# Optimization experiments

Measured on AMD Instinct MI355X. Metric: run time of the kernel, lower is better.

## Reference

```python
import jax, jax.numpy as jnp
import numpy as np


def setup_inputs() -> dict:
    key = jax.random.key(0)
    ks = jax.random.split(key, 6)
    B, H, T, Dk, Dv = 64, 16, 4, 128, 256
    q = jax.random.normal(ks[0], (B, H, T, Dk), dtype=jnp.float32)
    k = jax.random.normal(ks[1], (B, H, T, Dk), dtype=jnp.float32)
    v = jax.random.normal(ks[2], (B, H, T, Dv), dtype=jnp.float32)
    g = jax.random.uniform(ks[3], (B, H, T), dtype=jnp.float32)
    beta = jax.random.uniform(ks[4], (B, H, T), dtype=jnp.float32)
    last_recurrent_state = jax.random.normal(ks[5], (B, H, Dk, Dv), dtype=jnp.float32)
    return {"q": q, "k": k, "v": v, "g": g, "beta": beta,
            "last_recurrent_state": last_recurrent_state}


def reference(q, k, v, g, beta, last_recurrent_state):
    # q,k: (B,H,T,Dk)  v: (B,H,T,Dv)  g,beta: (B,H,T)  state: (B,H,Dk,Dv)
    def step(state, xs):
        q_t, k_t, v_t, g_t, beta_t = xs  # (B,H,Dk),(B,H,Dk),(B,H,Dv),(B,H),(B,H)
        state = state * jnp.exp(g_t)[..., None, None]           # decay
        kv_mem = jnp.einsum('bhkv,bhk->bhv', state, k_t)         # readout with key
        delta = (v_t - kv_mem) * beta_t[..., None]               # delta-rule correction
        state = state + k_t[..., None] * delta[..., None, :]     # rank-1 update
        out_t = jnp.einsum('bhkv,bhk->bhv', state, q_t)          # query readout
        return state, out_t

    xs = (jnp.moveaxis(q, 2, 0), jnp.moveaxis(k, 2, 0), jnp.moveaxis(v, 2, 0),
          jnp.moveaxis(g, 2, 0), jnp.moveaxis(beta, 2, 0))
    state, outs = jax.lax.scan(step, last_recurrent_state, xs)
    output = jnp.moveaxis(outs, 0, 2)  # (B,H,T,Dv)
    return jnp.concatenate([output.reshape(-1), state.reshape(-1)], axis=0)
```

## Files before the change

kernel.cpp:

```cpp
#include <hip/hip_runtime.h>

#define BH    1024
#define TT    4
#define DK    128
#define DV    256
#define KSEG  8
#define KLEN  16
#define HALFV 128
#define LDP   17

__global__ __launch_bounds__(256)
void delta_rule_kernel(const float* __restrict__ q,
                       const float* __restrict__ k,
                       const float* __restrict__ v,
                       const float* __restrict__ g,
                       const float* __restrict__ beta,
                       const float* __restrict__ s0,
                       float* __restrict__ out)
{
    const int bh   = blockIdx.x >> 1;
    const int half = blockIdx.x & 1;
    const int tid  = threadIdx.x;
    const int kg   = tid & (KSEG - 1);
    const int vg   = tid >> 3;
    const int vcol = half * HALFV + vg * 4;
    const int kr0  = kg * KLEN;

    const float* __restrict__ sin_p = s0 + (size_t)bh * DK * DV;
    float* __restrict__ out_p  = out + (size_t)bh * TT * DV;
    float* __restrict__ sout_p = out + (size_t)BH * TT * DV + (size_t)bh * DK * DV;

    const float* __restrict__ kbase = k    + (size_t)bh * TT * DK;
    const float* __restrict__ qbase = q    + (size_t)bh * TT * DK;
    const float* __restrict__ vbase = v    + (size_t)bh * TT * DV;
    const float* __restrict__ gbase = g    + (size_t)bh * TT;
    const float* __restrict__ bbase = beta + (size_t)bh * TT;

    __shared__ float ks[TT][KSEG * LDP];
    __shared__ float qs[TT][KSEG * LDP];

    const int i0 = tid;
    const int i1 = tid + 256;
    const float kl0 = kbase[i0];
    const float kl1 = kbase[i1];
    const float ql0 = qbase[i0];
    const float ql1 = qbase[i1];

    float4 s4[KLEN];
#pragma unroll
    for (int kk = 0; kk < KLEN; ++kk)
        s4[kk] = *(const float4*)&sin_p[(size_t)(kr0 + kk) * DV + vcol];

    {
        const int t0 = i0 >> 7, j0 = i0 & 127;
        const int t1 = i1 >> 7, j1 = i1 & 127;
        ks[t0][(j0 >> 4) * LDP + (j0 & 15)] = kl0;
        ks[t1][(j1 >> 4) * LDP + (j1 & 15)] = kl1;
        qs[t0][(j0 >> 4) * LDP + (j0 & 15)] = ql0;
        qs[t1][(j1 >> 4) * LDP + (j1 & 15)] = ql1;
    }
    __syncthreads();

#pragma unroll
    for (int t = 0; t < TT; ++t) {
        const float gt = expf(gbase[t]);
        const float bt = bbase[t];
        const float4 v4 = *(const float4*)&vbase[t * DV + vcol];

        float4 kv = make_float4(0.f, 0.f, 0.f, 0.f);
#pragma unroll
        for (int kk = 0; kk < KLEN; ++kk) {
            const float kt = ks[t][kg * LDP + kk];
            s4[kk].x *= gt; s4[kk].y *= gt; s4[kk].z *= gt; s4[kk].w *= gt;
            kv.x = fmaf(s4[kk].x, kt, kv.x);
            kv.y = fmaf(s4[kk].y, kt, kv.y);
            kv.z = fmaf(s4[kk].z, kt, kv.z);
            kv.w = fmaf(s4[kk].w, kt, kv.w);
        }
#pragma unroll
        for (int m = 1; m < KSEG; m <<= 1) {
            kv.x += __shfl_xor(kv.x, m);
            kv.y += __shfl_xor(kv.y, m);
            kv.z += __shfl_xor(kv.z, m);
            kv.w += __shfl_xor(kv.w, m);
        }

        float4 d4;
        d4.x = (v4.x - kv.x) * bt;
        d4.y = (v4.y - kv.y) * bt;
        d4.z = (v4.z - kv.z) * bt;
        d4.w = (v4.w - kv.w) * bt;

        float4 o4 = make_float4(0.f, 0.f, 0.f, 0.f);
#pragma unroll
        for (int kk = 0; kk < KLEN; ++kk) {
            const float kt = ks[t][kg * LDP + kk];
            const float qt = qs[t][kg * LDP + kk];
            s4[kk].x = fmaf(kt, d4.x, s4[kk].x);
            s4[kk].y = fmaf(kt, d4.y, s4[kk].y);
            s4[kk].z = fmaf(kt, d4.z, s4[kk].z);
            s4[kk].w = fmaf(kt, d4.w, s4[kk].w);
            o4.x = fmaf(s4[kk].x, qt, o4.x);
            o4.y = fmaf(s4[kk].y, qt, o4.y);
            o4.z = fmaf(s4[kk].z, qt, o4.z);
            o4.w = fmaf(s4[kk].w, qt, o4.w);
        }
#pragma unroll
        for (int m = 1; m < KSEG; m <<= 1) {
            o4.x += __shfl_xor(o4.x, m);
            o4.y += __shfl_xor(o4.y, m);
            o4.z += __shfl_xor(o4.z, m);
            o4.w += __shfl_xor(o4.w, m);
        }
        if (kg == 0)
            *(float4*)&out_p[t * DV + vcol] = o4;
    }

#pragma unroll
    for (int kk = 0; kk < KLEN; ++kk)
        *(float4*)&sout_p[(size_t)(kr0 + kk) * DV + vcol] = s4[kk];
}

extern "C" void kernel_launch(void* const* d_in, const int* in_sizes, int n_in,
                              void* d_out, int out_size, void* d_ws, size_t ws_size,
                              hipStream_t stream) {
    const float* q    = (const float*)d_in[0];
    const float* k    = (const float*)d_in[1];
    const float* v    = (const float*)d_in[2];
    const float* g    = (const float*)d_in[3];
    const float* beta = (const float*)d_in[4];
    const float* s0   = (const float*)d_in[5];
    float* out = (float*)d_out;

    delta_rule_kernel<<<dim3(BH * 2), dim3(256), 0, stream>>>(q, k, v, g, beta, s0, out);
}
```

Measured before the change: 258.8 us.

## Split Dv into quarters per block, prefetch v/g/beta, use nontemporal stores

Each (b,h) pair is now split across four blocks of 64 value columns instead of two, with 16 key segments of 8 rows per thread. This halves per-thread state registers and doubles the block count, giving more occupancy and parallelism. The v, g and beta loads are hoisted ahead of the time loop, and the output and state writes use nontemporal stores so they bypass the cache. In exchange, k and q are loaded redundantly by four blocks, and each reduction needs one more shuffle step.

```diff
diff --git a/kernel.cpp b/kernel.cpp
--- a/kernel.cpp
+++ b/kernel.cpp
@@ -4,10 +4,12 @@
 #define TT    4
 #define DK    128
 #define DV    256
-#define KSEG  8
-#define KLEN  16
-#define HALFV 128
-#define LDP   17
+#define KSEG  16
+#define KLEN  8
+#define QV    64
+#define LDP   9
+
+typedef float vfloat4 __attribute__((ext_vector_type(4)));
 
 __global__ __launch_bounds__(256)
 void delta_rule_kernel(const float* __restrict__ q,
@@ -18,12 +20,12 @@
                        const float* __restrict__ s0,
                        float* __restrict__ out)
 {
-    const int bh   = blockIdx.x >> 1;
-    const int half = blockIdx.x & 1;
+    const int bh      = blockIdx.x >> 2;
+    const int quarter = blockIdx.x & 3;
     const int tid  = threadIdx.x;
     const int kg   = tid & (KSEG - 1);
-    const int vg   = tid >> 3;
-    const int vcol = half * HALFV + vg * 4;
+    const int vg   = tid >> 4;
+    const int vcol = quarter * QV + vg * 4;
     const int kr0  = kg * KLEN;
 
     const float* __restrict__ sin_p = s0 + (size_t)bh * DK * DV;
@@ -46,6 +48,13 @@
     const float ql0 = qbase[i0];
     const float ql1 = qbase[i1];
 
+    const float4 gq = *(const float4*)&gbase[0];
+    const float4 bq = *(const float4*)&bbase[0];
+    float4 v4a[TT];
+#pragma unroll
+    for (int t = 0; t < TT; ++t)
+        v4a[t] = *(const float4*)&vbase[t * DV + vcol];
+
     float4 s4[KLEN];
 #pragma unroll
     for (int kk = 0; kk < KLEN; ++kk)
@@ -54,18 +63,21 @@
     {
         const int t0 = i0 >> 7, j0 = i0 & 127;
         const int t1 = i1 >> 7, j1 = i1 & 127;
-        ks[t0][(j0 >> 4) * LDP + (j0 & 15)] = kl0;
-        ks[t1][(j1 >> 4) * LDP + (j1 & 15)] = kl1;
-        qs[t0][(j0 >> 4) * LDP + (j0 & 15)] = ql0;
-        qs[t1][(j1 >> 4) * LDP + (j1 & 15)] = ql1;
+        ks[t0][(j0 >> 3) * LDP + (j0 & 7)] = kl0;
+        ks[t1][(j1 >> 3) * LDP + (j1 & 7)] = kl1;
+        qs[t0][(j0 >> 3) * LDP + (j0 & 7)] = ql0;
+        qs[t1][(j1 >> 3) * LDP + (j1 & 7)] = ql1;
     }
     __syncthreads();
 
+    const float garr[TT] = {gq.x, gq.y, gq.z, gq.w};
+    const float barr[TT] = {bq.x, bq.y, bq.z, bq.w};
+
 #pragma unroll
     for (int t = 0; t < TT; ++t) {
-        const float gt = expf(gbase[t]);
-        const float bt = bbase[t];
-        const float4 v4 = *(const float4*)&vbase[t * DV + vcol];
+        const float gt = expf(garr[t]);
+        const float bt = barr[t];
+        const float4 v4 = v4a[t];
 
         float4 kv = make_float4(0.f, 0.f, 0.f, 0.f);
 #pragma unroll
@@ -112,13 +124,18 @@
             o4.z += __shfl_xor(o4.z, m);
             o4.w += __shfl_xor(o4.w, m);
         }
-        if (kg == 0)
-            *(float4*)&out_p[t * DV + vcol] = o4;
+        if (kg == 0) {
+            vfloat4 ov = { o4.x, o4.y, o4.z, o4.w };
+            __builtin_nontemporal_store(ov, (vfloat4*)&out_p[t * DV + vcol]);
+        }
     }
 
 #pragma unroll
-    for (int kk = 0; kk < KLEN; ++kk)
-        *(float4*)&sout_p[(size_t)(kr0 + kk) * DV + vcol] = s4[kk];
+    for (int kk = 0; kk < KLEN; ++kk) {
+        vfloat4 sv = { s4[kk].x, s4[kk].y, s4[kk].z, s4[kk].w };
+        __builtin_nontemporal_store(sv,
+            (vfloat4*)&sout_p[(size_t)(kr0 + kk) * DV + vcol]);
+    }
 }
 
 extern "C" void kernel_launch(void* const* d_in, const int* in_sizes, int n_in,
@@ -132,5 +149,5 @@
     const float* s0   = (const float*)d_in[5];
     float* out = (float*)d_out;
 
-    delta_rule_kernel<<<dim3(BH * 2), dim3(256), 0, stream>>>(q, k, v, g, beta, s0, out);
+    delta_rule_kernel<<<dim3(BH * 4), dim3(256), 0, stream>>>(q, k, v, g, beta, s0, out);
 }
```

Result: slower. 276.1 us (+6.7%).
